# Optimization experiments

Hardware: AMD Instinct MI355X
Metric: run time of the kernel (lower is better)

The kernel has to match this reference:

```python
import jax, jax.numpy as jnp
import numpy as np

B, LQ, LKV, D, H = 4, 1024, 4096, 512, 4
HD = D // H  # head dim = 128


def setup_inputs() -> dict:
    key = jax.random.key(0)
    ks = jax.random.split(key, 6)
    s = 1.0 / np.sqrt(D)
    return {
        "x": jax.random.normal(ks[0], (B, LQ, D), jnp.float32),
        "encoder_feats": jax.random.normal(ks[1], (B, LKV, D), jnp.float32),
        "Wq": jax.random.normal(ks[2], (D, D), jnp.float32) * s,
        "Wk": jax.random.normal(ks[3], (D, D), jnp.float32) * s,
        "Wv": jax.random.normal(ks[4], (D, D), jnp.float32) * s,
        "bq": jnp.zeros((D,), jnp.float32),
        "bk": jnp.zeros((D,), jnp.float32),
        "bv": jnp.zeros((D,), jnp.float32),
        "Wo": jax.random.normal(ks[5], (D, D), jnp.float32) * s,
        "bo": jnp.zeros((D,), jnp.float32),
    }


def reference(x, encoder_feats, Wq, Wk, Wv, bq, bk, bv, Wo, bo):
    # nn.MultiheadAttention explicit (non-flash) path, dropout=0, eval.
    # Project, split heads: [B, L, D] -> [B, H, L, HD]
    def heads(t, L):
        return t.reshape(B, L, H, HD).transpose(0, 2, 1, 3)

    q = heads(x @ Wq.T + bq, LQ)
    k = heads(encoder_feats @ Wk.T + bk, LKV)
    v = heads(encoder_feats @ Wv.T + bv, LKV)

    scale = 1.0 / jnp.sqrt(jnp.asarray(HD, x.dtype))
    scores = jnp.einsum("bhqd,bhkd->bhqk", q, k) * scale  # [B,H,LQ,LKV]
    attn = jax.nn.softmax(scores, axis=-1)
    ctx = jnp.einsum("bhqk,bhkd->bhqd", attn, v)  # [B,H,LQ,HD]
    ctx = ctx.transpose(0, 2, 1, 3).reshape(B, LQ, D)
    attn_output = ctx @ Wo.T + bo
    # forward() returns attn_output only (fused/LayerNorm result is discarded)
    return attn_output
```

## Files before the change

### kernel.cpp

```cpp
#include <hip/hip_runtime.h>
#include <math.h>

#define B_    4
#define LQ_   1024
#define LKV_  4096
#define DM    512
#define NH    4
#define HD_   128

typedef _Float16 half8   __attribute__((ext_vector_type(8)));
typedef _Float16 half4_t __attribute__((ext_vector_type(4)));
typedef float    floatx4 __attribute__((ext_vector_type(4)));

#define MFMA16(a, b, c) __builtin_amdgcn_mfma_f32_16x16x32_f16((a), (b), (c), 0, 0, 0)

__global__ __launch_bounds__(256) void prep_cast(
    const float* __restrict__ x, const float* __restrict__ enc,
    const float* __restrict__ Wq, const float* __restrict__ Wk,
    const float* __restrict__ Wv, const float* __restrict__ Wo,
    _Float16* __restrict__ xh, _Float16* __restrict__ ench,
    _Float16* __restrict__ Wh)
{
  int i = blockIdx.x * 256 + threadIdx.x;
  const float* src; _Float16* dst; size_t off;
  if (i < 524288) { src = x; dst = xh; off = i; }
  else if (i < 2621440) { src = enc; dst = ench; off = i - 524288; }
  else {
    int j = i - 2621440;
    int wsel = j >> 16;
    src = (wsel == 0) ? Wq : (wsel == 1) ? Wk : (wsel == 2) ? Wv : Wo;
    dst = Wh + ((size_t)wsel << 18);
    off = j & 65535;
  }
  float4 v = *(const float4*)(src + off * 4);
  half4_t h;
  h[0] = (_Float16)v.x; h[1] = (_Float16)v.y;
  h[2] = (_Float16)v.z; h[3] = (_Float16)v.w;
  *(half4_t*)(dst + off * 4) = h;
}

template<int MODE>
__global__ __launch_bounds__(256) void proj_mfma(
    const _Float16* __restrict__ X,
    const _Float16* __restrict__ W,
    const float* __restrict__ bias,
    void* __restrict__ Yv, float scale)
{
  __shared__ _Float16 Xs[128][72];
  __shared__ _Float16 Ws[128][72];

  const int tid  = threadIdx.x;
  const int lane = tid & 63;
  const int w    = tid >> 6;
  const int n16  = lane & 15;
  const int quad = lane >> 4;
  const int wm   = (w & 1) * 64;
  const int wn   = (w >> 1) * 64;
  const int row0 = blockIdx.x * 128;
  const int col0 = blockIdx.y * 128;

  floatx4 acc[4][4];
#pragma unroll
  for (int a = 0; a < 4; ++a)
#pragma unroll
    for (int b = 0; b < 4; ++b) acc[a][b] = (floatx4){0.f, 0.f, 0.f, 0.f};

  for (int k0 = 0; k0 < 512; k0 += 64) {
#pragma unroll
    for (int i = 0; i < 4; ++i) {
      int c = i * 256 + tid;
      int r = c >> 3, off = (c & 7) * 8;
      *(half8*)&Xs[r][off] = *(const half8*)(X + (size_t)(row0 + r) * 512 + k0 + off);
      *(half8*)&Ws[r][off] = *(const half8*)(W + (size_t)(col0 + r) * 512 + k0 + off);
    }
    __syncthreads();
#pragma unroll
    for (int kc = 0; kc < 2; ++kc) {
      half8 af[4], bf[4];
#pragma unroll
      for (int mb = 0; mb < 4; ++mb)
        af[mb] = *(const half8*)&Xs[wm + mb * 16 + n16][kc * 32 + quad * 8];
#pragma unroll
      for (int nb = 0; nb < 4; ++nb)
        bf[nb] = *(const half8*)&Ws[wn + nb * 16 + n16][kc * 32 + quad * 8];
#pragma unroll
      for (int mb = 0; mb < 4; ++mb)
#pragma unroll
        for (int nb = 0; nb < 4; ++nb)
          acc[mb][nb] = MFMA16(af[mb], bf[nb], acc[mb][nb]);
    }
    __syncthreads();
  }

#pragma unroll
  for (int mb = 0; mb < 4; ++mb) {
#pragma unroll
    for (int nb = 0; nb < 4; ++nb) {
#pragma unroll
      for (int r = 0; r < 4; ++r) {
        int row = row0 + wm + mb * 16 + quad * 4 + r;
        int col = col0 + wn + nb * 16 + n16;
        float v = (acc[mb][nb][r] + bias[col]) * scale;
        if (MODE == 0) ((float*)Yv)[(size_t)row * 512 + col] = v;
        else ((_Float16*)Yv)[(size_t)row * 512 + col] = (_Float16)v;
      }
    }
  }
}

__global__ __launch_bounds__(256, 2) void proj_kv(
    const _Float16* __restrict__ Xe,
    const _Float16* __restrict__ Wk,
    const _Float16* __restrict__ Wv,
    const float* __restrict__ bk,
    const float* __restrict__ bv,
    _Float16* __restrict__ Kh,
    _Float16* __restrict__ Vt)
{
  __shared__ _Float16 SM[3 * 128 * 72];
  _Float16 (*Xs)[72]  = (_Float16(*)[72])SM;
  _Float16 (*Wks)[72] = (_Float16(*)[72])(SM + 128 * 72);
  _Float16 (*Wvs)[72] = (_Float16(*)[72])(SM + 2 * 128 * 72);

  const int tid  = threadIdx.x;
  const int lane = tid & 63;
  const int w    = tid >> 6;
  const int n16  = lane & 15;
  const int quad = lane >> 4;
  const int wm   = (w & 1) * 64;
  const int wn   = (w >> 1) * 64;
  const int row0 = blockIdx.x * 128;
  const int col0 = blockIdx.y * 128;

  floatx4 accK[4][4], accV[4][4];
#pragma unroll
  for (int a = 0; a < 4; ++a)
#pragma unroll
    for (int b = 0; b < 4; ++b) {
      accK[a][b] = (floatx4){0.f, 0.f, 0.f, 0.f};
      accV[a][b] = (floatx4){0.f, 0.f, 0.f, 0.f};
    }

  for (int k0 = 0; k0 < 512; k0 += 64) {
#pragma unroll
    for (int i = 0; i < 4; ++i) {
      int c = i * 256 + tid;
      int r = c >> 3, off = (c & 7) * 8;
      *(half8*)&Xs[r][off]  = *(const half8*)(Xe + (size_t)(row0 + r) * 512 + k0 + off);
      *(half8*)&Wks[r][off] = *(const half8*)(Wk + (size_t)(col0 + r) * 512 + k0 + off);
      *(half8*)&Wvs[r][off] = *(const half8*)(Wv + (size_t)(col0 + r) * 512 + k0 + off);
    }
    __syncthreads();
#pragma unroll
    for (int kc = 0; kc < 2; ++kc) {
      half8 af[4], bkf[4], bvf[4];
#pragma unroll
      for (int mb = 0; mb < 4; ++mb)
        af[mb] = *(const half8*)&Xs[wm + mb * 16 + n16][kc * 32 + quad * 8];
#pragma unroll
      for (int nb = 0; nb < 4; ++nb) {
        bkf[nb] = *(const half8*)&Wks[wn + nb * 16 + n16][kc * 32 + quad * 8];
        bvf[nb] = *(const half8*)&Wvs[wn + nb * 16 + n16][kc * 32 + quad * 8];
      }
#pragma unroll
      for (int mb = 0; mb < 4; ++mb)
#pragma unroll
        for (int nb = 0; nb < 4; ++nb) {
          accK[mb][nb] = MFMA16(af[mb], bkf[nb], accK[mb][nb]);
          accV[mb][nb] = MFMA16(af[mb], bvf[nb], accV[mb][nb]);
        }
    }
    __syncthreads();
  }

#pragma unroll
  for (int mb = 0; mb < 4; ++mb) {
#pragma unroll
    for (int nb = 0; nb < 4; ++nb) {
#pragma unroll
      for (int r = 0; r < 4; ++r) {
        int row = row0 + wm + mb * 16 + quad * 4 + r;
        int col = col0 + wn + nb * 16 + n16;
        Kh[(size_t)row * 512 + col] = (_Float16)(accK[mb][nb][r] + bk[col]);
      }
    }
  }

  _Float16 (*Ts)[144] = (_Float16(*)[144])SM;
#pragma unroll
  for (int mb = 0; mb < 4; ++mb) {
#pragma unroll
    for (int nb = 0; nb < 4; ++nb) {
      int dl = wn + nb * 16 + n16;
      float bi = bv[col0 + dl];
      half4_t hv;
#pragma unroll
      for (int r = 0; r < 4; ++r) hv[r] = (_Float16)(accV[mb][nb][r] + bi);
      *(half4_t*)&Ts[dl][wm + mb * 16 + quad * 4] = hv;
    }
  }
  __syncthreads();
  int b   = row0 >> 12;
  int kv0 = row0 & 4095;
#pragma unroll
  for (int i = 0; i < 8; ++i) {
    int f = i * 256 + tid;
    int dl = f >> 4, kv8 = (f & 15) * 8;
    half8 ov = *(const half8*)&Ts[dl][kv8];
    *(half8*)(Vt + (size_t)((b * 4 + blockIdx.y) * 128 + dl) * LKV_ + kv0 + kv8) = ov;
  }
}

__global__ __launch_bounds__(256, 2) void flash_mfma2(
    const _Float16* __restrict__ Qh,
    const _Float16* __restrict__ Kh,
    const _Float16* __restrict__ Vtg,
    _Float16* __restrict__ Opart,
    float* __restrict__ ml)
{
  __shared__ _Float16 U[4 * 32 * 72];
  __shared__ _Float16 Vs[128][72];
  _Float16 (*Ks)[136] = (_Float16(*)[136])U;
  _Float16* Ps = U;

  const int tid  = threadIdx.x;
  const int lane = tid & 63;
  const int w    = tid >> 6;
  const int n16  = lane & 15;
  const int quad = lane >> 4;

  const int xb    = blockIdx.x;
  const int qt    = blockIdx.y;
  const int split = xb & 7;
  const int bh    = xb >> 3;
  const int h = bh & 3, b = bh >> 2;

  const _Float16* Qg = Qh + (size_t)(b * LQ_ + qt * 128) * DM + h * HD_;
  const _Float16* Kg = Kh + (size_t)(b * LKV_) * DM + h * HD_;
  const _Float16* Vg = Vtg + (size_t)(bh * HD_) * LKV_;

  half8 qf[2][4];
  const int chunk = w >> 1;
  const int qrb   = (w & 1) * 32;
#pragma unroll
  for (int c = 0; c < 2; ++c) {
#pragma unroll
    for (int i = 0; i < 4; ++i) {
      int f = i * 256 + tid;
      int r = f >> 4, c8 = (f & 15) * 8;
      *(half8*)&Ks[r][c8] = *(const half8*)(Qg + (size_t)(c * 64 + r) * DM + c8);
    }
    __syncthreads();
    if (chunk == c) {
#pragma unroll
      for (int qb = 0; qb < 2; ++qb)
#pragma unroll
        for (int kc = 0; kc < 4; ++kc)
          qf[qb][kc] = *(const half8*)&Ks[qrb + qb * 16 + n16][kc * 32 + quad * 8];
    }
    __syncthreads();
  }

  floatx4 o[2][8];
#pragma unroll
  for (int mb = 0; mb < 2; ++mb)
#pragma unroll
    for (int vb = 0; vb < 8; ++vb) o[mb][vb] = (floatx4){0.f, 0.f, 0.f, 0.f};
  float m_i[2] = {-INFINITY, -INFINITY};
  float l_i[2] = {0.f, 0.f};

  for (int kt = split * 8; kt < split * 8 + 8; ++kt) {
#pragma unroll
    for (int i = 0; i < 4; ++i) {
      int f = i * 256 + tid;
      int r = f >> 4, c8 = (f & 15) * 8;
      *(half8*)&Ks[r][c8] = *(const half8*)(Kg + (size_t)(kt * 64 + r) * DM + c8);
    }
#pragma unroll
    for (int i = 0; i < 4; ++i) {
      int f = i * 256 + tid;
      int d = f >> 3, kv8 = (f & 7) * 8;
      *(half8*)&Vs[d][kv8] = *(const half8*)(Vg + (size_t)d * LKV_ + kt * 64 + kv8);
    }
    __syncthreads();

    floatx4 s[2][4];
#pragma unroll
    for (int qb = 0; qb < 2; ++qb)
#pragma unroll
      for (int cb = 0; cb < 4; ++cb) s[qb][cb] = (floatx4){0.f, 0.f, 0.f, 0.f};
#pragma unroll
    for (int cb = 0; cb < 4; ++cb) {
#pragma unroll
      for (int kc = 0; kc < 4; ++kc) {
        half8 kf = *(const half8*)&Ks[cb * 16 + n16][kc * 32 + quad * 8];
        s[0][cb] = MFMA16(kf, qf[0][kc], s[0][cb]);
        s[1][cb] = MFMA16(kf, qf[1][kc], s[1][cb]);
      }
    }
    __syncthreads();

    float alpha[2];
#pragma unroll
    for (int qb = 0; qb < 2; ++qb) {
      float mx = -INFINITY;
#pragma unroll
      for (int cb = 0; cb < 4; ++cb)
#pragma unroll
        for (int r = 0; r < 4; ++r) mx = fmaxf(mx, s[qb][cb][r]);
      mx = fmaxf(mx, __shfl_xor(mx, 16));
      mx = fmaxf(mx, __shfl_xor(mx, 32));
      float mn = fmaxf(m_i[qb], mx);
      alpha[qb] = __expf(m_i[qb] - mn);
      m_i[qb] = mn;
      float rs = 0.f;
#pragma unroll
      for (int cb = 0; cb < 4; ++cb) {
        half4_t ph;
#pragma unroll
        for (int r = 0; r < 4; ++r) {
          float p = __expf(s[qb][cb][r] - mn);
          rs += p;
          ph[r] = (_Float16)p;
        }
        *(half4_t*)&Ps[(w * 32 + qb * 16 + n16) * 72 + cb * 16 + quad * 4] = ph;
      }
      rs += __shfl_xor(rs, 16);
      rs += __shfl_xor(rs, 32);
      l_i[qb] = l_i[qb] * alpha[qb] + rs;
    }

#pragma unroll
    for (int mb = 0; mb < 2; ++mb) {
#pragma unroll
      for (int r = 0; r < 4; ++r) {
        float a = __shfl(alpha[mb], (lane & 48) | (quad * 4 + r));
#pragma unroll
        for (int vb = 0; vb < 8; ++vb) o[mb][vb][r] *= a;
      }
    }

    half8 pf[2][2];
#pragma unroll
    for (int mb = 0; mb < 2; ++mb)
#pragma unroll
      for (int kc = 0; kc < 2; ++kc)
        pf[mb][kc] = *(const half8*)&Ps[(w * 32 + mb * 16 + n16) * 72 + kc * 32 + quad * 8];
#pragma unroll
    for (int vb = 0; vb < 8; ++vb) {
#pragma unroll
      for (int kc = 0; kc < 2; ++kc) {
        half8 vf = *(const half8*)&Vs[vb * 16 + n16][kc * 32 + quad * 8];
        o[0][vb] = MFMA16(pf[0][kc], vf, o[0][vb]);
        o[1][vb] = MFMA16(pf[1][kc], vf, o[1][vb]);
      }
    }
    __syncthreads();
  }

  _Float16* Og = Opart + ((size_t)xb * 1024 + qt * 128 + w * 32) * HD_;
#pragma unroll
  for (int mb = 0; mb < 2; ++mb) {
#pragma unroll
    for (int r = 0; r < 4; ++r) {
#pragma unroll
      for (int vb = 0; vb < 8; ++vb)
        Og[(size_t)(mb * 16 + quad * 4 + r) * HD_ + vb * 16 + n16] =
            (_Float16)o[mb][vb][r];
    }
  }
  if (quad == 0) {
#pragma unroll
    for (int qb = 0; qb < 2; ++qb) {
      size_t qi = (size_t)xb * 1024 + qt * 128 + w * 32 + qb * 16 + n16;
      ml[qi * 2] = m_i[qb];
      ml[qi * 2 + 1] = l_i[qb];
    }
  }
}

__global__ __launch_bounds__(256) void combine_splits(
    const _Float16* __restrict__ Opart,
    const float* __restrict__ ml,
    _Float16* __restrict__ CTXh)
{
  int g  = blockIdx.x * 2 + (threadIdx.x >> 7);
  int d  = threadIdx.x & 127;
  int bh = g >> 10, q = g & 1023;
  int b = bh >> 2, h = bh & 3;

  float m[8], l[8], M = -INFINITY;
#pragma unroll
  for (int p = 0; p < 8; ++p) {
    size_t idx = ((size_t)(bh * 8 + p) * 1024 + q) * 2;
    m[p] = ml[idx]; l[p] = ml[idx + 1];
    M = fmaxf(M, m[p]);
  }
  float L = 0.f, o = 0.f;
#pragma unroll
  for (int p = 0; p < 8; ++p) {
    float wgt = __expf(m[p] - M);
    L += wgt * l[p];
    o += wgt * (float)Opart[((size_t)(bh * 8 + p) * 1024 + q) * HD_ + d];
  }
  CTXh[(size_t)(b * LQ_ + q) * DM + h * HD_ + d] = (_Float16)(o / L);
}

extern "C" void kernel_launch(void* const* d_in, const int* in_sizes, int n_in,
                              void* d_out, int out_size, void* d_ws, size_t ws_size,
                              hipStream_t stream) {
  const float* x   = (const float*)d_in[0];
  const float* enc = (const float*)d_in[1];
  const float* Wq  = (const float*)d_in[2];
  const float* Wk  = (const float*)d_in[3];
  const float* Wv  = (const float*)d_in[4];
  const float* bq  = (const float*)d_in[5];
  const float* bk  = (const float*)d_in[6];
  const float* bv  = (const float*)d_in[7];
  const float* Wo  = (const float*)d_in[8];
  const float* bo  = (const float*)d_in[9];
  float* out = (float*)d_out;

  char* ws = (char*)d_ws;
  _Float16* Qh    = (_Float16*)(ws);
  _Float16* Kh    = (_Float16*)(ws + (4u  << 20));
  _Float16* Vtg   = (_Float16*)(ws + (20u << 20));
  _Float16* ench  = (_Float16*)(ws + (36u << 20));
  _Float16* xh    = (_Float16*)(ws + (52u << 20));
  _Float16* Opart = (_Float16*)(ws + (36u << 20));
  _Float16* CTXh  = (_Float16*)(ws + (68u << 20));
  float*    mlp   = (float*)   (ws + (72u << 20));
  _Float16* Wh    = (_Float16*)(ws + (73u << 20));

  _Float16* Whq = Wh;
  _Float16* Whk = Wh + 262144;
  _Float16* Whv = Wh + 524288;
  _Float16* Who = Wh + 786432;

  const float qscale = 0.08838834764831845f;
  dim3 blk(256);

  prep_cast<<<dim3(11264), blk, 0, stream>>>(x, enc, Wq, Wk, Wv, Wo, xh, ench, Wh);

  proj_mfma<1><<<dim3(32, 4), blk, 0, stream>>>(xh, Whq, bq, Qh, qscale);
  proj_kv<<<dim3(128, 4), blk, 0, stream>>>(ench, Whk, Whv, bk, bv, Kh, Vtg);

  flash_mfma2<<<dim3(128, 8), blk, 0, stream>>>(Qh, Kh, Vtg, Opart, mlp);

  combine_splits<<<dim3(8192), blk, 0, stream>>>(Opart, mlp, CTXh);

  proj_mfma<0><<<dim3(32, 4), blk, 0, stream>>>(CTXh, Who, bo, out, 1.f);
}
```

Baseline: 212.7 us.

## Fuse fp32 cast into QKV projection, merge Q/KV launches, halve flash splits

The separate fp32-to-fp16 cast of x and encoder features is removed. The projection kernels now load fp32 directly and convert while staging into shared memory, and the Q and KV projections are merged into one launch with a blockIdx-based branch. The flash kernel's KV split count drops from 8 to 4, which doubles the work per block and halves the combine traffic. The output rescale is skipped when a wavefront-wide ballot shows alpha is 1. Together these cut intermediate global traffic and launches, at the cost of fewer flash blocks (512) and possibly less occupancy.

```diff
diff --git a/kernel.cpp b/kernel.cpp
--- a/kernel.cpp
+++ b/kernel.cpp
@@ -14,40 +14,40 @@
 
 #define MFMA16(a, b, c) __builtin_amdgcn_mfma_f32_16x16x32_f16((a), (b), (c), 0, 0, 0)
 
-__global__ __launch_bounds__(256) void prep_cast(
-    const float* __restrict__ x, const float* __restrict__ enc,
+__global__ __launch_bounds__(256) void prep_w(
     const float* __restrict__ Wq, const float* __restrict__ Wk,
     const float* __restrict__ Wv, const float* __restrict__ Wo,
-    _Float16* __restrict__ xh, _Float16* __restrict__ ench,
     _Float16* __restrict__ Wh)
 {
   int i = blockIdx.x * 256 + threadIdx.x;
-  const float* src; _Float16* dst; size_t off;
-  if (i < 524288) { src = x; dst = xh; off = i; }
-  else if (i < 2621440) { src = enc; dst = ench; off = i - 524288; }
-  else {
-    int j = i - 2621440;
-    int wsel = j >> 16;
-    src = (wsel == 0) ? Wq : (wsel == 1) ? Wk : (wsel == 2) ? Wv : Wo;
-    dst = Wh + ((size_t)wsel << 18);
-    off = j & 65535;
-  }
+  int wsel = i >> 16;
+  const float* src = (wsel == 0) ? Wq : (wsel == 1) ? Wk : (wsel == 2) ? Wv : Wo;
+  size_t off = i & 65535;
   float4 v = *(const float4*)(src + off * 4);
   half4_t h;
   h[0] = (_Float16)v.x; h[1] = (_Float16)v.y;
   h[2] = (_Float16)v.z; h[3] = (_Float16)v.w;
-  *(half4_t*)(dst + off * 4) = h;
+  *(half4_t*)(Wh + ((size_t)wsel << 18) + off * 4) = h;
 }
 
-template<int MODE>
-__global__ __launch_bounds__(256) void proj_mfma(
-    const _Float16* __restrict__ X,
-    const _Float16* __restrict__ W,
-    const float* __restrict__ bias,
-    void* __restrict__ Yv, float scale)
+__global__ __launch_bounds__(256, 2) void proj_qkv(
+    const float* __restrict__ x,
+    const float* __restrict__ enc,
+    const _Float16* __restrict__ Whq,
+    const _Float16* __restrict__ Whk,
+    const _Float16* __restrict__ Whv,
+    const float* __restrict__ bq,
+    const float* __restrict__ bk,
+    const float* __restrict__ bv,
+    _Float16* __restrict__ Qh,
+    _Float16* __restrict__ Kh,
+    _Float16* __restrict__ Vt,
+    float qscale)
 {
-  __shared__ _Float16 Xs[128][72];
-  __shared__ _Float16 Ws[128][72];
+  __shared__ _Float16 SM[3 * 128 * 72];
+  _Float16 (*Xs)[72]  = (_Float16(*)[72])SM;
+  _Float16 (*Ws1)[72] = (_Float16(*)[72])(SM + 128 * 72);
+  _Float16 (*Ws2)[72] = (_Float16(*)[72])(SM + 2 * 128 * 72);
 
   const int tid  = threadIdx.x;
   const int lane = tid & 63;
@@ -56,111 +56,100 @@
   const int quad = lane >> 4;
   const int wm   = (w & 1) * 64;
   const int wn   = (w >> 1) * 64;
-  const int row0 = blockIdx.x * 128;
   const int col0 = blockIdx.y * 128;
 
-  floatx4 acc[4][4];
+  if ((int)blockIdx.x >= 128) {
+    const int row0 = ((int)blockIdx.x - 128) * 128;
+    floatx4 acc[4][4];
+#pragma unroll
+    for (int a = 0; a < 4; ++a)
+#pragma unroll
+      for (int b = 0; b < 4; ++b) acc[a][b] = (floatx4){0.f, 0.f, 0.f, 0.f};
+
+    for (int k0 = 0; k0 < 512; k0 += 64) {
+#pragma unroll
+      for (int i = 0; i < 4; ++i) {
+        int c = i * 256 + tid;
+        int r = c >> 3, off = (c & 7) * 8;
+        const float* xp = x + (size_t)(row0 + r) * 512 + k0 + off;
+        float4 a = *(const float4*)xp, b2 = *(const float4*)(xp + 4);
+        half8 hx;
+        hx[0] = (_Float16)a.x;  hx[1] = (_Float16)a.y;
+        hx[2] = (_Float16)a.z;  hx[3] = (_Float16)a.w;
+        hx[4] = (_Float16)b2.x; hx[5] = (_Float16)b2.y;
+        hx[6] = (_Float16)b2.z; hx[7] = (_Float16)b2.w;
+        *(half8*)&Xs[r][off] = hx;
+        *(half8*)&Ws1[r][off] = *(const half8*)(Whq + (size_t)(col0 + r) * 512 + k0 + off);
+      }
+      __syncthreads();
+#pragma unroll
+      for (int kc = 0; kc < 2; ++kc) {
+        half8 af[4], bf[4];
+#pragma unroll
+        for (int mb = 0; mb < 4; ++mb)
+          af[mb] = *(const half8*)&Xs[wm + mb * 16 + n16][kc * 32 + quad * 8];
+#pragma unroll
+        for (int nb = 0; nb < 4; ++nb)
+          bf[nb] = *(const half8*)&Ws1[wn + nb * 16 + n16][kc * 32 + quad * 8];
+#pragma unroll
+        for (int mb = 0; mb < 4; ++mb)
+#pragma unroll
+          for (int nb = 0; nb < 4; ++nb)
+            acc[mb][nb] = MFMA16(af[mb], bf[nb], acc[mb][nb]);
+      }
+      __syncthreads();
+    }
+#pragma unroll
+    for (int mb = 0; mb < 4; ++mb)
+#pragma unroll
+      for (int nb = 0; nb < 4; ++nb)
+#pragma unroll
+        for (int r = 0; r < 4; ++r) {
+          int row = row0 + wm + mb * 16 + quad * 4 + r;
+          int col = col0 + wn + nb * 16 + n16;
+          Qh[(size_t)row * 512 + col] =
+              (_Float16)((acc[mb][nb][r] + bq[col]) * qscale);
+        }
+    return;
+  }
+
+  const int row0 = (int)blockIdx.x * 128;
+  floatx4 accK[4][4], accV[4][4];
 #pragma unroll
   for (int a = 0; a < 4; ++a)
 #pragma unroll
-    for (int b = 0; b < 4; ++b) acc[a][b] = (floatx4){0.f, 0.f, 0.f, 0.f};
+    for (int b = 0; b < 4; ++b) {
+      accK[a][b] = (floatx4){0.f, 0.f, 0.f, 0.f};
+      accV[a][b] = (floatx4){0.f, 0.f, 0.f, 0.f};
+    }
 
   for (int k0 = 0; k0 < 512; k0 += 64) {
 #pragma unroll
     for (int i = 0; i < 4; ++i) {
       int c = i * 256 + tid;
       int r = c >> 3, off = (c & 7) * 8;
-      *(half8*)&Xs[r][off] = *(const half8*)(X + (size_t)(row0 + r) * 512 + k0 + off);
-      *(half8*)&Ws[r][off] = *(const half8*)(W + (size_t)(col0 + r) * 512 + k0 + off);
+      const float* xp = enc + (size_t)(row0 + r) * 512 + k0 + off;
+      float4 a = *(const float4*)xp, b2 = *(const float4*)(xp + 4);
+      half8 hx;
+      hx[0] = (_Float16)a.x;  hx[1] = (_Float16)a.y;
+      hx[2] = (_Float16)a.z;  hx[3] = (_Float16)a.w;
+      hx[4] = (_Float16)b2.x; hx[5] = (_Float16)b2.y;
+      hx[6] = (_Float16)b2.z; hx[7] = (_Float16)b2.w;
+      *(half8*)&Xs[r][off] = hx;
+      *(half8*)&Ws1[r][off] = *(const half8*)(Whk + (size_t)(col0 + r) * 512 + k0 + off);
+      *(half8*)&Ws2[r][off] = *(const half8*)(Whv + (size_t)(col0 + r) * 512 + k0 + off);
     }
     __syncthreads();
 #pragma unroll
     for (int kc = 0; kc < 2; ++kc) {
-      half8 af[4], bf[4];
+      half8 af[4], bkf[4], bvf[4];
 #pragma unroll
       for (int mb = 0; mb < 4; ++mb)
         af[mb] = *(const half8*)&Xs[wm + mb * 16 + n16][kc * 32 + quad * 8];
 #pragma unroll
-      for (int nb = 0; nb < 4; ++nb)
-        bf[nb] = *(const half8*)&Ws[wn + nb * 16 + n16][kc * 32 + quad * 8];
-#pragma unroll
-      for (int mb = 0; mb < 4; ++mb)
-#pragma unroll
-        for (int nb = 0; nb < 4; ++nb)
-          acc[mb][nb] = MFMA16(af[mb], bf[nb], acc[mb][nb]);
-    }
-    __syncthreads();
-  }
-
-#pragma unroll
-  for (int mb = 0; mb < 4; ++mb) {
-#pragma unroll
-    for (int nb = 0; nb < 4; ++nb) {
-#pragma unroll
-      for (int r = 0; r < 4; ++r) {
-        int row = row0 + wm + mb * 16 + quad * 4 + r;
-        int col = col0 + wn + nb * 16 + n16;
-        float v = (acc[mb][nb][r] + bias[col]) * scale;
-        if (MODE == 0) ((float*)Yv)[(size_t)row * 512 + col] = v;
-        else ((_Float16*)Yv)[(size_t)row * 512 + col] = (_Float16)v;
-      }
-    }
-  }
-}
-
-__global__ __launch_bounds__(256, 2) void proj_kv(
-    const _Float16* __restrict__ Xe,
-    const _Float16* __restrict__ Wk,
-    const _Float16* __restrict__ Wv,
-    const float* __restrict__ bk,
-    const float* __restrict__ bv,
-    _Float16* __restrict__ Kh,
-    _Float16* __restrict__ Vt)
-{
-  __shared__ _Float16 SM[3 * 128 * 72];
-  _Float16 (*Xs)[72]  = (_Float16(*)[72])SM;
-  _Float16 (*Wks)[72] = (_Float16(*)[72])(SM + 128 * 72);
-  _Float16 (*Wvs)[72] = (_Float16(*)[72])(SM + 2 * 128 * 72);
-
-  const int tid  = threadIdx.x;
-  const int lane = tid & 63;
-  const int w    = tid >> 6;
-  const int n16  = lane & 15;
-  const int quad = lane >> 4;
-  const int wm   = (w & 1) * 64;
-  const int wn   = (w >> 1) * 64;
-  const int row0 = blockIdx.x * 128;
-  const int col0 = blockIdx.y * 128;
-
-  floatx4 accK[4][4], accV[4][4];
-#pragma unroll
-  for (int a = 0; a < 4; ++a)
-#pragma unroll
-    for (int b = 0; b < 4; ++b) {
-      accK[a][b] = (floatx4){0.f, 0.f, 0.f, 0.f};
-      accV[a][b] = (floatx4){0.f, 0.f, 0.f, 0.f};
-    }
-
-  for (int k0 = 0; k0 < 512; k0 += 64) {
-#pragma unroll
-    for (int i = 0; i < 4; ++i) {
-      int c = i * 256 + tid;
-      int r = c >> 3, off = (c & 7) * 8;
-      *(half8*)&Xs[r][off]  = *(const half8*)(Xe + (size_t)(row0 + r) * 512 + k0 + off);
-      *(half8*)&Wks[r][off] = *(const half8*)(Wk + (size_t)(col0 + r) * 512 + k0 + off);
-      *(half8*)&Wvs[r][off] = *(const half8*)(Wv + (size_t)(col0 + r) * 512 + k0 + off);
-    }
-    __syncthreads();
-#pragma unroll
-    for (int kc = 0; kc < 2; ++kc) {
-      half8 af[4], bkf[4], bvf[4];
-#pragma unroll
-      for (int mb = 0; mb < 4; ++mb)
-        af[mb] = *(const half8*)&Xs[wm + mb * 16 + n16][kc * 32 + quad * 8];
-#pragma unroll
       for (int nb = 0; nb < 4; ++nb) {
-        bkf[nb] = *(const half8*)&Wks[wn + nb * 16 + n16][kc * 32 + quad * 8];
-        bvf[nb] = *(const half8*)&Wvs[wn + nb * 16 + n16][kc * 32 + quad * 8];
+        bkf[nb] = *(const half8*)&Ws1[wn + nb * 16 + n16][kc * 32 + quad * 8];
+        bvf[nb] = *(const half8*)&Ws2[wn + nb * 16 + n16][kc * 32 + quad * 8];
       }
 #pragma unroll
       for (int mb = 0; mb < 4; ++mb)
@@ -174,21 +163,19 @@
   }
 
 #pragma unroll
-  for (int mb = 0; mb < 4; ++mb) {
-#pragma unroll
-    for (int nb = 0; nb < 4; ++nb) {
+  for (int mb = 0; mb < 4; ++mb)
+#pragma unroll
+    for (int nb = 0; nb < 4; ++nb)
 #pragma unroll
       for (int r = 0; r < 4; ++r) {
         int row = row0 + wm + mb * 16 + quad * 4 + r;
         int col = col0 + wn + nb * 16 + n16;
         Kh[(size_t)row * 512 + col] = (_Float16)(accK[mb][nb][r] + bk[col]);
       }
-    }
-  }
 
   _Float16 (*Ts)[144] = (_Float16(*)[144])SM;
 #pragma unroll
-  for (int mb = 0; mb < 4; ++mb) {
+  for (int mb = 0; mb < 4; ++mb)
 #pragma unroll
     for (int nb = 0; nb < 4; ++nb) {
       int dl = wn + nb * 16 + n16;
@@ -198,7 +185,6 @@
       for (int r = 0; r < 4; ++r) hv[r] = (_Float16)(accV[mb][nb][r] + bi);
       *(half4_t*)&Ts[dl][wm + mb * 16 + quad * 4] = hv;
     }
-  }
   __syncthreads();
   int b   = row0 >> 12;
   int kv0 = row0 & 4095;
@@ -231,8 +217,8 @@
 
   const int xb    = blockIdx.x;
   const int qt    = blockIdx.y;
-  const int split = xb & 7;
-  const int bh    = xb >> 3;
+  const int split = xb & 3;
+  const int bh    = xb >> 2;
   const int h = bh & 3, b = bh >> 2;
 
   const _Float16* Qg = Qh + (size_t)(b * LQ_ + qt * 128) * DM + h * HD_;
@@ -269,7 +255,7 @@
   float m_i[2] = {-INFINITY, -INFINITY};
   float l_i[2] = {0.f, 0.f};
 
-  for (int kt = split * 8; kt < split * 8 + 8; ++kt) {
+  for (int kt = split * 16; kt < split * 16 + 16; ++kt) {
 #pragma unroll
     for (int i = 0; i < 4; ++i) {
       int f = i * 256 + tid;
@@ -330,13 +316,15 @@
       l_i[qb] = l_i[qb] * alpha[qb] + rs;
     }
 
-#pragma unroll
-    for (int mb = 0; mb < 2; ++mb) {
-#pragma unroll
-      for (int r = 0; r < 4; ++r) {
-        float a = __shfl(alpha[mb], (lane & 48) | (quad * 4 + r));
-#pragma unroll
-        for (int vb = 0; vb < 8; ++vb) o[mb][vb][r] *= a;
+    if (__ballot((alpha[0] != 1.f) || (alpha[1] != 1.f))) {
+#pragma unroll
+      for (int mb = 0; mb < 2; ++mb) {
+#pragma unroll
+        for (int r = 0; r < 4; ++r) {
+          float a = __shfl(alpha[mb], (lane & 48) | (quad * 4 + r));
+#pragma unroll
+          for (int vb = 0; vb < 8; ++vb) o[mb][vb][r] *= a;
+        }
       }
     }
 
@@ -360,15 +348,13 @@
 
   _Float16* Og = Opart + ((size_t)xb * 1024 + qt * 128 + w * 32) * HD_;
 #pragma unroll
-  for (int mb = 0; mb < 2; ++mb) {
-#pragma unroll
-    for (int r = 0; r < 4; ++r) {
+  for (int mb = 0; mb < 2; ++mb)
+#pragma unroll
+    for (int r = 0; r < 4; ++r)
 #pragma unroll
       for (int vb = 0; vb < 8; ++vb)
         Og[(size_t)(mb * 16 + quad * 4 + r) * HD_ + vb * 16 + n16] =
             (_Float16)o[mb][vb][r];
-    }
-  }
   if (quad == 0) {
 #pragma unroll
     for (int qb = 0; qb < 2; ++qb) {
@@ -389,21 +375,85 @@
   int bh = g >> 10, q = g & 1023;
   int b = bh >> 2, h = bh & 3;
 
-  float m[8], l[8], M = -INFINITY;
-#pragma unroll
-  for (int p = 0; p < 8; ++p) {
-    size_t idx = ((size_t)(bh * 8 + p) * 1024 + q) * 2;
+  float m[4], l[4], M = -INFINITY;
+#pragma unroll
+  for (int p = 0; p < 4; ++p) {
+    size_t idx = ((size_t)(bh * 4 + p) * 1024 + q) * 2;
     m[p] = ml[idx]; l[p] = ml[idx + 1];
     M = fmaxf(M, m[p]);
   }
   float L = 0.f, o = 0.f;
 #pragma unroll
-  for (int p = 0; p < 8; ++p) {
+  for (int p = 0; p < 4; ++p) {
     float wgt = __expf(m[p] - M);
     L += wgt * l[p];
-    o += wgt * (float)Opart[((size_t)(bh * 8 + p) * 1024 + q) * HD_ + d];
+    o += wgt * (float)Opart[((size_t)(bh * 4 + p) * 1024 + q) * HD_ + d];
   }
   CTXh[(size_t)(b * LQ_ + q) * DM + h * HD_ + d] = (_Float16)(o / L);
+}
+
+__global__ __launch_bounds__(256) void proj_out(
+    const _Float16* __restrict__ X,
+    const _Float16* __restrict__ W,
+    const float* __restrict__ bias,
+    float* __restrict__ Y)
+{
+  __shared__ _Float16 Xs[128][72];
+  __shared__ _Float16 Ws[128][72];
+
+  const int tid  = threadIdx.x;
+  const int lane = tid & 63;
+  const int w    = tid >> 6;
+  const int n16  = lane & 15;
+  const int quad = lane >> 4;
+  const int wm   = (w & 1) * 64;
+  const int wn   = (w >> 1) * 64;
+  const int row0 = blockIdx.x * 128;
+  const int col0 = blockIdx.y * 128;
+
+  floatx4 acc[4][4];
+#pragma unroll
+  for (int a = 0; a < 4; ++a)
+#pragma unroll
+    for (int b = 0; b < 4; ++b) acc[a][b] = (floatx4){0.f, 0.f, 0.f, 0.f};
+
+  for (int k0 = 0; k0 < 512; k0 += 64) {
+#pragma unroll
+    for (int i = 0; i < 4; ++i) {
+      int c = i * 256 + tid;
+      int r = c >> 3, off = (c & 7) * 8;
+      *(half8*)&Xs[r][off] = *(const half8*)(X + (size_t)(row0 + r) * 512 + k0 + off);
+      *(half8*)&Ws[r][off] = *(const half8*)(W + (size_t)(col0 + r) * 512 + k0 + off);
+    }
+    __syncthreads();
+#pragma unroll
+    for (int kc = 0; kc < 2; ++kc) {
+      half8 af[4], bf[4];
+#pragma unroll
+      for (int mb = 0; mb < 4; ++mb)
+        af[mb] = *(const half8*)&Xs[wm + mb * 16 + n16][kc * 32 + quad * 8];
+#pragma unroll
+      for (int nb = 0; nb < 4; ++nb)
+        bf[nb] = *(const half8*)&Ws[wn + nb * 16 + n16][kc * 32 + quad * 8];
+#pragma unroll
+      for (int mb = 0; mb < 4; ++mb)
+#pragma unroll
+        for (int nb = 0; nb < 4; ++nb)
+          acc[mb][nb] = MFMA16(af[mb], bf[nb], acc[mb][nb]);
+    }
+    __syncthreads();
+  }
+
+#pragma unroll
+  for (int mb = 0; mb < 4; ++mb)
+#pragma unroll
+    for (int nb = 0; nb < 4; ++nb)
+#pragma unroll
+      for (int r = 0; r < 4; ++r) {
+        int row = row0 + wm + mb * 16 + quad * 4 + r;
+        int col = col0 + wn + nb * 16 + n16;
+        Y[(size_t)row * 512 + col] = acc[mb][nb][r] + bias[col];
+      }
 }
 
 extern "C" void kernel_launch(void* const* d_in, const int* in_sizes, int n_in,
@@ -425,12 +475,10 @@
   _Float16* Qh    = (_Float16*)(ws);
   _Float16* Kh    = (_Float16*)(ws + (4u  << 20));
   _Float16* Vtg   = (_Float16*)(ws + (20u << 20));
-  _Float16* ench  = (_Float16*)(ws + (36u << 20));
-  _Float16* xh    = (_Float16*)(ws + (52u << 20));
   _Float16* Opart = (_Float16*)(ws + (36u << 20));
-  _Float16* CTXh  = (_Float16*)(ws + (68u << 20));
-  float*    mlp   = (float*)   (ws + (72u << 20));
-  _Float16* Wh    = (_Float16*)(ws + (73u << 20));
+  _Float16* CTXh  = (_Float16*)(ws + (52u << 20));
+  float*    mlp   = (float*)   (ws + (56u << 20));
+  _Float16* Wh    = (_Float16*)(ws + (57u << 20));
 
   _Float16* Whq = Wh;
   _Float16* Whk = Wh + 262144;
@@ -440,14 +488,14 @@
   const float qscale = 0.08838834764831845f;
   dim3 blk(256);
 
-  prep_cast<<<dim3(11264), blk, 0, stream>>>(x, enc, Wq, Wk, Wv, Wo, xh, ench, Wh);
-
-  proj_mfma<1><<<dim3(32, 4), blk, 0, stream>>>(xh, Whq, bq, Qh, qscale);
-  proj_kv<<<dim3(128, 4), blk, 0, stream>>>(ench, Whk, Whv, bk, bv, Kh, Vtg);
-
-  flash_mfma2<<<dim3(128, 8), blk, 0, stream>>>(Qh, Kh, Vtg, Opart, mlp);
+  prep_w<<<dim3(1024), blk, 0, stream>>>(Wq, Wk, Wv, Wo, Wh);
+
+  proj_qkv<<<dim3(160, 4), blk, 0, stream>>>(
+      x, enc, Whq, Whk, Whv, bq, bk, bv, Qh, Kh, Vtg, qscale);
+
+  flash_mfma2<<<dim3(64, 8), blk, 0, stream>>>(Qh, Kh, Vtg, Opart, mlp);
 
   combine_splits<<<dim3(8192), blk, 0, stream>>>(Opart, mlp, CTXh);
 
-  proj_mfma<0><<<dim3(32, 4), blk, 0, stream>>>(CTXh, Who, bo, out, 1.f);
+  proj_out<<<dim3(32, 4), blk, 0, stream>>>(CTXh, Who, bo, out);
 }
```

New measurement: 202.3 us. 1.05x faster.
